# Performance work log

Measured on AMD Instinct MI355X. Metric: run time of the kernel, lower is better.

Reference implementation:

```python
import jax, jax.numpy as jnp
import numpy as np

B, S, D = 2, 2048, 4096
H, KVH, HD = 32, 8, 128
N_REP = H // KVH
ROPE_THETA = 10000.0


def setup_inputs() -> dict:
    key = jax.random.key(0)
    ks = jax.random.split(key, 6)
    x_norm = jax.random.normal(ks[0], (B, S, D), dtype=jnp.float32)
    scale = 0.02
    wq = jax.random.normal(ks[1], (H * HD, D), dtype=jnp.float32) * scale
    wk = jax.random.normal(ks[2], (KVH * HD, D), dtype=jnp.float32) * scale
    wv = jax.random.normal(ks[3], (KVH * HD, D), dtype=jnp.float32) * scale
    wo = jax.random.normal(ks[4], (D, H * HD), dtype=jnp.float32) * scale
    # RoPE tables: freqs_cis[t, j] = exp(i * t * theta^{-2j/HD})
    inv_freq = 1.0 / (ROPE_THETA ** (jnp.arange(0, HD, 2, dtype=jnp.float32) / HD))  # [HD/2]
    angles = jnp.arange(S, dtype=jnp.float32)[:, None] * inv_freq[None, :]  # [S, HD/2]
    freqs_cos = jnp.cos(angles)
    freqs_sin = jnp.sin(angles)
    # causal additive mask (0 on/below diagonal, -1e9 above)
    mask = jnp.where(jnp.arange(S)[None, :] > jnp.arange(S)[:, None], jnp.float32(-1e9), jnp.float32(0.0))
    return {"x_norm": x_norm, "wq": wq, "wk": wk, "wv": wv, "wo": wo,
            "freqs_cos": freqs_cos, "freqs_sin": freqs_sin, "mask": mask, "start_pos": 0}


def _apply_rope(t, cos, sin):
    # t: [B, S, h, HD]; cos/sin: [S, HD/2] -> rotate consecutive pairs
    tr = t.reshape(*t.shape[:-1], HD // 2, 2)
    t0, t1 = tr[..., 0], tr[..., 1]
    c = cos[None, :, None, :]
    s = sin[None, :, None, :]
    out = jnp.stack([t0 * c - t1 * s, t0 * s + t1 * c], axis=-1)
    return out.reshape(t.shape)


def reference(x_norm, wq, wk, wv, wo, freqs_cos, freqs_sin, mask, start_pos):
    # QKV projections (torch Linear: y = x @ W.T)
    xq = jnp.einsum("bsd,ed->bse", x_norm, wq).reshape(B, S, H, HD)
    xk = jnp.einsum("bsd,ed->bse", x_norm, wk).reshape(B, S, KVH, HD)
    xv = jnp.einsum("bsd,ed->bse", x_norm, wv).reshape(B, S, KVH, HD)
    xq = _apply_rope(xq, freqs_cos, freqs_sin)
    xk = _apply_rope(xk, freqs_cos, freqs_sin)
    # start_pos == 0 prefill: cache slice [:start_pos+seqlen] == freshly written xk/xv
    keys = jnp.repeat(xk, N_REP, axis=2)    # [B, S, H, HD] (GQA repeat_kv)
    values = jnp.repeat(xv, N_REP, axis=2)  # [B, S, H, HD]
    scale = 1.0 / np.sqrt(HD).astype(np.float32)
    scores = jnp.einsum("bqhd,bkhd->bhqk", xq, keys) * scale
    scores = scores + mask[None, None, :, :]
    probs = jax.nn.softmax(scores.astype(jnp.float32), axis=-1).astype(xq.dtype)
    out = jnp.einsum("bhqk,bkhd->bqhd", probs, values).reshape(B, S, H * HD)
    return jnp.einsum("bse,de->bsd", out, wo)
```

## Files before the change

kernel.cpp:

```cpp
#include <hip/hip_runtime.h>
#include <stdint.h>

#define B_N 2
#define S_N 2048
#define D_N 4096
#define H_N 32
#define KVH_N 8
#define HD_N 128
#define NQT (S_N / 64)
#define QS_LOG2E 0.12751743f

typedef __attribute__((ext_vector_type(8))) short bf16x8;
typedef __attribute__((ext_vector_type(4))) float f32x4;

__device__ __forceinline__ unsigned short f2bf(float f) {
    union { float f; unsigned u; } v; v.f = f;
    unsigned u = v.u;
    u += 0x7fffu + ((u >> 16) & 1u);
    return (unsigned short)(u >> 16);
}
__device__ __forceinline__ float bf2f(unsigned short h) {
    union { unsigned u; float f; } v; v.u = ((unsigned)h) << 16;
    return v.f;
}
__device__ __forceinline__ unsigned cvt_pk_bf16(float lo, float hi) {
    unsigned r;
    asm("v_cvt_pk_bf16_f32 %0, %1, %2" : "=v"(r) : "v"(lo), "v"(hi));
    return r;
}

__device__ __forceinline__ void gl16(const unsigned short* g, unsigned short* l) {
    __builtin_amdgcn_global_load_lds(
        (const __attribute__((address_space(1))) void*)g,
        (__attribute__((address_space(3))) void*)l, 16, 0, 0);
}

__global__ void __launch_bounds__(256) conv_f32_bf16(const float* __restrict__ in,
                                                     unsigned short* __restrict__ out) {
    int i = (blockIdx.x * 256 + threadIdx.x) * 4;
    float4 v = *(const float4*)(in + i);
    ushort4 o;
    o.x = f2bf(v.x); o.y = f2bf(v.y); o.z = f2bf(v.z); o.w = f2bf(v.w);
    *(ushort4*)(out + i) = o;
}

template<int HEADS, int STRIDE>
__global__ void __launch_bounds__(256) rope_kernel(unsigned short* __restrict__ t,
                                                   const float* __restrict__ cosb,
                                                   const float* __restrict__ sinb,
                                                   float scale) {
    int p = blockIdx.x * 256 + threadIdx.x;
    int i = p & 63;
    int hr = p >> 6;
    int m = hr / HEADS;
    int hh = hr - m * HEADS;
    int s = m & (S_N - 1);
    size_t off = (size_t)m * STRIDE + hh * HD_N + 2 * i;
    unsigned v = *(const unsigned*)(t + off);
    float t0 = bf2f((unsigned short)(v & 0xffffu));
    float t1 = bf2f((unsigned short)(v >> 16));
    float c = cosb[s * 64 + i], sn = sinb[s * 64 + i];
    float o0 = (t0 * c - t1 * sn) * scale;
    float o1 = (t0 * sn + t1 * c) * scale;
    *(unsigned*)(t + off) = (unsigned)f2bf(o0) | ((unsigned)f2bf(o1) << 16);
}

#define BAR() __builtin_amdgcn_s_barrier()
#define VMC4() asm volatile("s_waitcnt vmcnt(4)" ::: "memory")

#define STG(SRC, LDSBUF, H, T) do {                                         \
        int kk_ = ((T) * 64) & kmask;                                       \
        gl16(SRC[(H)*2 + 0] + kk_, &LDSBUF[((H)*2 + 0) * 4096 + dstoff]);   \
        gl16(SRC[(H)*2 + 1] + kk_, &LDSBUF[((H)*2 + 1) * 4096 + dstoff]);   \
    } while (0)

template<int F32OUT>
__global__ void __launch_bounds__(512, 2)
gemm256(const unsigned short* __restrict__ A, const unsigned short* __restrict__ Bm,
        void* __restrict__ Cv, int M, int N, int K) {
    __shared__ unsigned short ldsA[2][16384];
    __shared__ unsigned short ldsB[2][16384];

    const int tid = threadIdx.x;
    const int lane = tid & 63;
    const int w = tid >> 6;
    const int li = lane & 15, lg = lane >> 4;
    const int wr = w >> 2, wc = w & 3;

    const int nwg = gridDim.x;
    const int cpx = nwg >> 3;
    const int wg = (blockIdx.x & 7) * cpx + (blockIdx.x >> 3);
    const int nbn = N >> 8;
    const int bm = wg / nbn, bn = wg - bm * nbn;
    const int m0 = bm << 8, n0 = bn << 8;

    const int rbase = ((tid >> 7) << 4) + ((tid >> 2) & 15);
    const int cstg = ((tid >> 6) & 1) * 32 + (((tid & 3) * 8) ^ (((tid >> 5) & 1) << 4));
    const unsigned short* Asrc[4];
    const unsigned short* Bsrc[4];
#pragma unroll
    for (int hj = 0; hj < 4; ++hj) {
        Asrc[hj] = A + (size_t)(m0 + hj * 64 + rbase) * K + cstg;
        Bsrc[hj] = Bm + (size_t)(n0 + hj * 64 + rbase) * K + cstg;
    }
    const int dstoff = tid * 8;
    const int kmask = K - 1;

    f32x4 acc[8][4];
#pragma unroll
    for (int i = 0; i < 8; ++i)
#pragma unroll
        for (int j = 0; j < 4; ++j) acc[i][j] = (f32x4){0.f, 0.f, 0.f, 0.f};

    const int colpart = (lg * 16) ^ ((li >> 3) << 5);

#define LDB(buf) do {                                                        \
        _Pragma("unroll")                                                    \
        for (int ni_ = 0; ni_ < 4; ++ni_) {                                  \
            _Pragma("unroll")                                                \
            for (int ks_ = 0; ks_ < 2; ++ks_)                                \
                bfr[ni_][ks_] = *(const bf16x8*)((const char*)&ldsB[buf][0]  \
                    + (wc * 4 + ni_) * 2048 + ks_ * 1024 + li * 64 + colpart); \
        }                                                                    \
    } while (0)

#define LDA(buf, q) do {                                                     \
        _Pragma("unroll")                                                    \
        for (int m_ = 0; m_ < 2; ++m_) {                                     \
            _Pragma("unroll")                                                \
            for (int ks_ = 0; ks_ < 2; ++ks_)                                \
                af[m_][ks_] = *(const bf16x8*)((const char*)&ldsA[buf][0]    \
                    + (wr * 8 + (q) * 2 + m_) * 2048 + ks_ * 1024 + li * 64 + colpart); \
        }                                                                    \
    } while (0)

#define MFMAQ(q) do {                                                        \
        __builtin_amdgcn_s_setprio(1);                                       \
        _Pragma("unroll")                                                    \
        for (int ks_ = 0; ks_ < 2; ++ks_) {                                  \
            _Pragma("unroll")                                                \
            for (int m_ = 0; m_ < 2; ++m_) {                                 \
                _Pragma("unroll")                                            \
                for (int ni_ = 0; ni_ < 4; ++ni_)                            \
                    acc[(q)*2 + m_][ni_] = __builtin_amdgcn_mfma_f32_16x16x32_bf16( \
                        af[m_][ks_], bfr[ni_][ks_], acc[(q)*2 + m_][ni_], 0, 0, 0); \
            }                                                                \
        }                                                                    \
        __builtin_amdgcn_s_setprio(0);                                       \
    } while (0)

    STG(Asrc, ldsA[0], 0, 0); STG(Asrc, ldsA[0], 1, 0);
    STG(Bsrc, ldsB[0], 0, 0); STG(Bsrc, ldsB[0], 1, 0);
    STG(Bsrc, ldsB[1], 0, 1); STG(Bsrc, ldsB[1], 1, 1);
    VMC4();
    BAR();

    const int NIT = K >> 7;
    bf16x8 bfr[4][2], af[2][2];
#pragma unroll 1
    for (int i = 0; i < NIT; ++i) {
        const int T = 2 * i;
        LDB(0); LDA(0, 0);
        STG(Asrc, ldsA[1], 0, T + 1);
        BAR(); MFMAQ(0); BAR();
        LDA(0, 1);
        STG(Asrc, ldsA[1], 1, T + 1);
        STG(Bsrc, ldsB[0], 0, T + 2);
        BAR(); MFMAQ(1); BAR();
        LDA(0, 2);
        STG(Bsrc, ldsB[0], 1, T + 2);
        BAR(); MFMAQ(2); BAR();
        LDA(0, 3);
        BAR(); MFMAQ(3); VMC4(); BAR();
        LDB(1); LDA(1, 0);
        STG(Asrc, ldsA[0], 0, T + 2);
        BAR(); MFMAQ(0); BAR();
        LDA(1, 1);
        STG(Asrc, ldsA[0], 1, T + 2);
        BAR(); MFMAQ(1); BAR();
        LDA(1, 2);
        STG(Bsrc, ldsB[1], 0, T + 3);
        BAR(); MFMAQ(2); BAR();
        LDA(1, 3);
        STG(Bsrc, ldsB[1], 1, T + 3);
        BAR(); MFMAQ(3); VMC4(); BAR();
    }

    const int r0 = m0 + wr * 128 + lg * 4;
    const int c0 = n0 + wc * 64 + li;
    if (F32OUT) {
        float* C = (float*)Cv;
#pragma unroll
        for (int mi = 0; mi < 8; ++mi)
#pragma unroll
            for (int ni = 0; ni < 4; ++ni)
#pragma unroll
                for (int rr = 0; rr < 4; ++rr)
                    C[(size_t)(r0 + mi * 16 + rr) * N + c0 + ni * 16] = acc[mi][ni][rr];
    } else {
        unsigned short* C = (unsigned short*)Cv;
#pragma unroll
        for (int mi = 0; mi < 8; ++mi)
#pragma unroll
            for (int ni = 0; ni < 4; ++ni)
#pragma unroll
                for (int rr = 0; rr < 4; ++rr)
                    C[(size_t)(r0 + mi * 16 + rr) * N + c0 + ni * 16] = f2bf(acc[mi][ni][rr]);
    }
#undef LDB
#undef LDA
#undef MFMAQ
}


__device__ __forceinline__ void stage_k8(const unsigned short* kt_base,
                                         unsigned short* ks_base, int w, int lane) {
#pragma unroll
    for (int j = 0; j < 2; ++j) {
        int row = (w * 2 + j) * 4 + (lane >> 4);
        int colb = (lane & 15) * 16;
        int key = (row & 7) << 4;
        gl16(kt_base + (size_t)row * 2048 + ((colb ^ key) >> 1),
             ks_base + (w * 2 + j) * 512);
    }
}

__device__ __forceinline__ void load_v(const unsigned short* vt_base, int tid, uint4& a0, uint4& a1) {
    int kv = (tid >> 4) * 2, d0 = (tid & 15) * 8;
    const unsigned short* vp = vt_base + (size_t)kv * 2048 + d0;
    a0 = *(const uint4*)vp;
    a1 = *(const uint4*)(vp + 2048);
}

__device__ __forceinline__ void write_v(unsigned short* vt_lds, int tid, uint4 a0, uint4 a1) {
    int kv = (tid >> 4) * 2, d0 = (tid & 15) * 8;
    union { uint4 q; unsigned short u[8]; } x0, x1;
    x0.q = a0; x1.q = a1;
#pragma unroll
    for (int jj = 0; jj < 8; ++jj) {
        int d = d0 + jj;
        unsigned pack = (unsigned)x0.u[jj] | ((unsigned)x1.u[jj] << 16);
        int key = ((d ^ (d >> 3)) & 7) << 4;
        *(unsigned*)((char*)vt_lds + d * 128 + ((kv * 2) ^ key)) = pack;
    }
}

__global__ void __launch_bounds__(512, 2) attn_kernel(const unsigned short* __restrict__ Q,
                                                      const unsigned short* __restrict__ Kb,
                                                      const unsigned short* __restrict__ Vb,
                                                      unsigned short* __restrict__ O) {
    __shared__ unsigned short Ks[2][64 * 128];
    __shared__ unsigned short Vt[2][128 * 64];

    const int pidx = blockIdx.x;
    const int bg = blockIdx.y;
    const int b = bg >> 3, kvh = bg & 7;
    const int tid = threadIdx.x;
    const int w = tid >> 6, lane = tid & 63;
    const int li = lane & 15, lg = lane >> 4;
    const int h = kvh * 4 + (w >> 1);
    const int qh = (w & 1) * 32;

    const unsigned short* KVrow0 = Kb + (size_t)b * S_N * 2048 + kvh * 128;
    const unsigned short* Vrow0  = Vb + (size_t)b * S_N * 2048 + kvh * 128;

#pragma unroll 1
    for (int pass = 0; pass < 2; ++pass) {
        const int qt = pass ? (NQT - 1 - pidx) : pidx;
        const int nt = qt + 1;

        bf16x8 qf[2][4];
        {
            const unsigned short* qp = Q + ((size_t)b * S_N + qt * 64 + qh + li) * (H_N * HD_N)
                                         + h * HD_N + lg * 8;
#pragma unroll
            for (int mi = 0; mi < 2; ++mi)
#pragma unroll
                for (int ds = 0; ds < 4; ++ds)
                    qf[mi][ds] = *(const bf16x8*)(qp + (size_t)mi * 16 * (H_N * HD_N) + ds * 32);
        }

        float mreg[2], lreg[2];
#pragma unroll
        for (int mi = 0; mi < 2; ++mi) { mreg[mi] = -1e30f; lreg[mi] = 0.f; }
        f32x4 o_acc[2][8];
#pragma unroll
        for (int mi = 0; mi < 2; ++mi)
#pragma unroll
            for (int di = 0; di < 8; ++di) o_acc[mi][di] = (f32x4){0.f, 0.f, 0.f, 0.f};

        {
            stage_k8(KVrow0, &Ks[0][0], w, lane);
            uint4 a0, a1;
            load_v(Vrow0, tid, a0, a1);
            write_v(&Vt[0][0], tid, a0, a1);
        }
        __syncthreads();

#pragma unroll 1
        for (int t = 0; t < nt; ++t) {
            const int c = t & 1;
            const bool pre = (t + 1 < nt);
            uint4 a0, a1;
            if (pre) {
                stage_k8(KVrow0 + (size_t)(t + 1) * 64 * 2048, &Ks[c ^ 1][0], w, lane);
                load_v(Vrow0 + (size_t)(t + 1) * 64 * 2048, tid, a0, a1);
            }

            f32x4 sT[2][4];
#pragma unroll
            for (int mi = 0; mi < 2; ++mi)
#pragma unroll
                for (int ni = 0; ni < 4; ++ni) sT[mi][ni] = (f32x4){0.f, 0.f, 0.f, 0.f};
            __builtin_amdgcn_s_setprio(1);
#pragma unroll
            for (int ni = 0; ni < 4; ++ni) {
                const int kvc = ni * 16 + li;
                const int kkey = (kvc & 7) << 4;
                bf16x8 kf[4];
#pragma unroll
                for (int ds = 0; ds < 4; ++ds)
                    kf[ds] = *(const bf16x8*)((char*)&Ks[c][0] + kvc * 256
                                              + ((ds * 64 + lg * 16) ^ kkey));
#pragma unroll
                for (int mi = 0; mi < 2; ++mi)
#pragma unroll
                    for (int ds = 0; ds < 4; ++ds)
                        sT[mi][ni] = __builtin_amdgcn_mfma_f32_16x16x32_bf16(kf[ds], qf[mi][ds], sT[mi][ni], 0, 0, 0);
            }
            __builtin_amdgcn_s_setprio(0);

            if (t == qt) {
#pragma unroll
                for (int mi = 0; mi < 2; ++mi) {
                    int qq = qh + mi * 16 + li;
#pragma unroll
                    for (int ni = 0; ni < 4; ++ni)
#pragma unroll
                        for (int r = 0; r < 4; ++r)
                            if (ni * 16 + lg * 4 + r > qq) sT[mi][ni][r] = -1e30f;
                }
            }

            float fac0[2];
#pragma unroll
            for (int mi = 0; mi < 2; ++mi) {
                float pm = sT[mi][0][0];
#pragma unroll
                for (int ni = 0; ni < 4; ++ni)
#pragma unroll
                    for (int r = 0; r < 4; ++r) pm = fmaxf(pm, sT[mi][ni][r]);
                pm = fmaxf(pm, __shfl_xor(pm, 16));
                pm = fmaxf(pm, __shfl_xor(pm, 32));
                float mn = fmaxf(mreg[mi], pm);
                fac0[mi] = __builtin_amdgcn_exp2f(mreg[mi] - mn);
                mreg[mi] = mn;
#pragma unroll
                for (int ni = 0; ni < 4; ++ni)
#pragma unroll
                    for (int r = 0; r < 4; ++r)
                        sT[mi][ni][r] = __builtin_amdgcn_exp2f(sT[mi][ni][r] - mn);
                float rs = 0.f;
#pragma unroll
                for (int ni = 0; ni < 4; ++ni)
#pragma unroll
                    for (int r = 0; r < 4; ++r) rs += sT[mi][ni][r];
                rs += __shfl_xor(rs, 16);
                rs += __shfl_xor(rs, 32);
                lreg[mi] = lreg[mi] * fac0[mi] + rs;
            }

#pragma unroll
            for (int mi = 0; mi < 2; ++mi) {
                float facR[4];
#pragma unroll
                for (int rr = 0; rr < 4; ++rr)
                    facR[rr] = __shfl(fac0[mi], (lg << 4) | (lg * 4 + rr));
#pragma unroll
                for (int di = 0; di < 8; ++di)
#pragma unroll
                    for (int rr = 0; rr < 4; ++rr) o_acc[mi][di][rr] *= facR[rr];
            }

            union U { bf16x8 v; unsigned u[4]; };
            U pa[2][2];
#pragma unroll
            for (int mi = 0; mi < 2; ++mi)
#pragma unroll
                for (int ks = 0; ks < 2; ++ks) {
                    pa[mi][ks].u[0] = cvt_pk_bf16(sT[mi][2 * ks][0], sT[mi][2 * ks][1]);
                    pa[mi][ks].u[1] = cvt_pk_bf16(sT[mi][2 * ks][2], sT[mi][2 * ks][3]);
                    pa[mi][ks].u[2] = cvt_pk_bf16(sT[mi][2 * ks + 1][0], sT[mi][2 * ks + 1][1]);
                    pa[mi][ks].u[3] = cvt_pk_bf16(sT[mi][2 * ks + 1][2], sT[mi][2 * ks + 1][3]);
                }

            __builtin_amdgcn_s_setprio(1);
#pragma unroll
            for (int di = 0; di < 8; ++di) {
                int d = di * 16 + li;
                int vkey = ((d ^ (d >> 3)) & 7) << 4;
                const char* vbase = (const char*)&Vt[c][0] + d * 128;
                bf16x8 vf[2];
#pragma unroll
                for (int ks = 0; ks < 2; ++ks) {
                    union { bf16x8 v; unsigned long long g[2]; } vv;
                    int cb = ks * 64 + lg * 8;
                    vv.g[0] = *(const unsigned long long*)(vbase + (cb ^ vkey));
                    vv.g[1] = *(const unsigned long long*)(vbase + ((cb + 32) ^ vkey));
                    vf[ks] = vv.v;
                }
#pragma unroll
                for (int mi = 0; mi < 2; ++mi)
#pragma unroll
                    for (int ks = 0; ks < 2; ++ks)
                        o_acc[mi][di] = __builtin_amdgcn_mfma_f32_16x16x32_bf16(pa[mi][ks].v, vf[ks], o_acc[mi][di], 0, 0, 0);
            }
            __builtin_amdgcn_s_setprio(0);

            if (pre) write_v(&Vt[c ^ 1][0], tid, a0, a1);
            __syncthreads();
        }

        unsigned short* op = O + ((size_t)b * S_N + qt * 64 + qh + lg * 4) * (H_N * HD_N)
                               + h * HD_N + li;
#pragma unroll
        for (int mi = 0; mi < 2; ++mi) {
            float iv = 1.f / lreg[mi];
            float ivR[4];
#pragma unroll
            for (int rr = 0; rr < 4; ++rr)
                ivR[rr] = __shfl(iv, (lg << 4) | (lg * 4 + rr));
#pragma unroll
            for (int di = 0; di < 8; ++di)
#pragma unroll
                for (int rr = 0; rr < 4; ++rr)
                    op[((size_t)(mi * 16 + rr)) * (H_N * HD_N) + di * 16]
                        = f2bf(o_acc[mi][di][rr] * ivR[rr]);
        }
    }
}

extern "C" void kernel_launch(void* const* d_in, const int* in_sizes, int n_in,
                              void* d_out, int out_size, void* d_ws, size_t ws_size,
                              hipStream_t stream) {
    (void)in_sizes; (void)n_in; (void)out_size; (void)ws_size;
    const float* x  = (const float*)d_in[0];
    const float* wq = (const float*)d_in[1];
    const float* wk = (const float*)d_in[2];
    const float* wv = (const float*)d_in[3];
    const float* wo = (const float*)d_in[4];
    const float* fc = (const float*)d_in[5];
    const float* fs = (const float*)d_in[6];
    float* out = (float*)d_out;

    char* ws = (char*)d_ws;
    unsigned short* xb  = (unsigned short*)(ws);
    unsigned short* wb  = (unsigned short*)(ws + 33554432);
    unsigned short* wkv = (unsigned short*)(ws + 67108864);
    unsigned short* Qb  = (unsigned short*)(ws + 83886080);
    unsigned short* KVb = (unsigned short*)(ws + 117440512);

    const int BS = B_N * S_N;

    conv_f32_bf16<<<dim3(BS * D_N / 1024), 256, 0, stream>>>(x, xb);
    conv_f32_bf16<<<dim3(H_N * HD_N * D_N / 1024), 256, 0, stream>>>(wq, wb);
    conv_f32_bf16<<<dim3(KVH_N * HD_N * D_N / 1024), 256, 0, stream>>>(wk, wkv);
    conv_f32_bf16<<<dim3(KVH_N * HD_N * D_N / 1024), 256, 0, stream>>>(wv, wkv + KVH_N * HD_N * D_N);

    gemm256<0><<<dim3((BS / 256) * (D_N / 256)), 512, 0, stream>>>(xb, wb, Qb, BS, D_N, D_N);
    conv_f32_bf16<<<dim3(D_N * H_N * HD_N / 1024), 256, 0, stream>>>(wo, wb);
    gemm256<0><<<dim3((BS / 256) * (2048 / 256)), 512, 0, stream>>>(xb, wkv, KVb, BS, 2048, D_N);

    rope_kernel<H_N, H_N * HD_N><<<dim3(BS * H_N * 64 / 256), 256, 0, stream>>>(Qb, fc, fs, QS_LOG2E);
    rope_kernel<KVH_N, 2 * KVH_N * HD_N><<<dim3(BS * KVH_N * 64 / 256), 256, 0, stream>>>(KVb, fc, fs, 1.0f);

    attn_kernel<<<dim3(NQT / 2, B_N * KVH_N), 512, 0, stream>>>(Qb, KVb, KVb + 1024, Qb);

    gemm256<1><<<dim3((BS / 256) * (D_N / 256)), 512, 0, stream>>>(Qb, wb, out, BS, D_N, D_N);
}
```

Measured before the change: 594.2 us.

## Double-buffer GEMM LDS fragments in registers to overlap reads with MFMA

Restructures the gemm256 main loop so A/B fragments are read from LDS into a second register set while MFMAs run on the first. This removes one of the two barriers per quarter step, so each step has one barrier instead of a barrier before and after the MFMA block. It also replaces the per-row source pointer arrays with a single base pointer plus computed offsets to save registers. The cost is more fragment registers, which may pressure occupancy under the 512x2 launch bounds. It also risks LDS write/read hazards now that fewer barriers separate staging from fragment reads.

```diff
diff --git a/kernel.cpp b/kernel.cpp
--- a/kernel.cpp
+++ b/kernel.cpp
@@ -68,12 +68,6 @@
 #define BAR() __builtin_amdgcn_s_barrier()
 #define VMC4() asm volatile("s_waitcnt vmcnt(4)" ::: "memory")
 
-#define STG(SRC, LDSBUF, H, T) do {                                         \
-        int kk_ = ((T) * 64) & kmask;                                       \
-        gl16(SRC[(H)*2 + 0] + kk_, &LDSBUF[((H)*2 + 0) * 4096 + dstoff]);   \
-        gl16(SRC[(H)*2 + 1] + kk_, &LDSBUF[((H)*2 + 1) * 4096 + dstoff]);   \
-    } while (0)
-
 template<int F32OUT>
 __global__ void __launch_bounds__(512, 2)
 gemm256(const unsigned short* __restrict__ A, const unsigned short* __restrict__ Bm,
@@ -96,13 +90,8 @@
 
     const int rbase = ((tid >> 7) << 4) + ((tid >> 2) & 15);
     const int cstg = ((tid >> 6) & 1) * 32 + (((tid & 3) * 8) ^ (((tid >> 5) & 1) << 4));
-    const unsigned short* Asrc[4];
-    const unsigned short* Bsrc[4];
-#pragma unroll
-    for (int hj = 0; hj < 4; ++hj) {
-        Asrc[hj] = A + (size_t)(m0 + hj * 64 + rbase) * K + cstg;
-        Bsrc[hj] = Bm + (size_t)(n0 + hj * 64 + rbase) * K + cstg;
-    }
+    const unsigned short* Abase = A + (size_t)(m0 + rbase) * K + cstg;
+    const unsigned short* Bbase = Bm + (size_t)(n0 + rbase) * K + cstg;
     const int dstoff = tid * 8;
     const int kmask = K - 1;
 
@@ -114,76 +103,99 @@
 
     const int colpart = (lg * 16) ^ ((li >> 3) << 5);
 
-#define LDB(buf) do {                                                        \
-        _Pragma("unroll")                                                    \
-        for (int ni_ = 0; ni_ < 4; ++ni_) {                                  \
-            _Pragma("unroll")                                                \
-            for (int ks_ = 0; ks_ < 2; ++ks_)                                \
-                bfr[ni_][ks_] = *(const bf16x8*)((const char*)&ldsB[buf][0]  \
-                    + (wc * 4 + ni_) * 2048 + ks_ * 1024 + li * 64 + colpart); \
-        }                                                                    \
+#define STG(BASE, LDSBUF, H, T) do {                                              \
+        int kk_ = ((T) * 64) & kmask;                                             \
+        gl16(BASE + (size_t)(((H) * 2 + 0) * 64) * K + kk_,                       \
+             &LDSBUF[((H) * 2 + 0) * 4096 + dstoff]);                             \
+        gl16(BASE + (size_t)(((H) * 2 + 1) * 64) * K + kk_,                       \
+             &LDSBUF[((H) * 2 + 1) * 4096 + dstoff]);                             \
     } while (0)
 
-#define LDA(buf, q) do {                                                     \
-        _Pragma("unroll")                                                    \
-        for (int m_ = 0; m_ < 2; ++m_) {                                     \
-            _Pragma("unroll")                                                \
-            for (int ks_ = 0; ks_ < 2; ++ks_)                                \
-                af[m_][ks_] = *(const bf16x8*)((const char*)&ldsA[buf][0]    \
+#define LDBs(set, buf) do {                                                       \
+        _Pragma("unroll")                                                         \
+        for (int ni_ = 0; ni_ < 4; ++ni_) {                                       \
+            _Pragma("unroll")                                                     \
+            for (int ks_ = 0; ks_ < 2; ++ks_)                                     \
+                bfr[set][ni_][ks_] = *(const bf16x8*)((const char*)&ldsB[buf][0]  \
+                    + (wc * 4 + ni_) * 2048 + ks_ * 1024 + li * 64 + colpart);    \
+        }                                                                         \
+    } while (0)
+
+#define LDAs(set, buf, q) do {                                                    \
+        _Pragma("unroll")                                                         \
+        for (int m_ = 0; m_ < 2; ++m_) {                                          \
+            _Pragma("unroll")                                                     \
+            for (int ks_ = 0; ks_ < 2; ++ks_)                                     \
+                af[set][m_][ks_] = *(const bf16x8*)((const char*)&ldsA[buf][0]    \
                     + (wr * 8 + (q) * 2 + m_) * 2048 + ks_ * 1024 + li * 64 + colpart); \
-        }                                                                    \
+        }                                                                         \
     } while (0)
 
-#define MFMAQ(q) do {                                                        \
-        __builtin_amdgcn_s_setprio(1);                                       \
-        _Pragma("unroll")                                                    \
-        for (int ks_ = 0; ks_ < 2; ++ks_) {                                  \
-            _Pragma("unroll")                                                \
-            for (int m_ = 0; m_ < 2; ++m_) {                                 \
-                _Pragma("unroll")                                            \
-                for (int ni_ = 0; ni_ < 4; ++ni_)                            \
-                    acc[(q)*2 + m_][ni_] = __builtin_amdgcn_mfma_f32_16x16x32_bf16( \
-                        af[m_][ks_], bfr[ni_][ks_], acc[(q)*2 + m_][ni_], 0, 0, 0); \
-            }                                                                \
-        }                                                                    \
-        __builtin_amdgcn_s_setprio(0);                                       \
+#define MFMAs(sb, sa, q) do {                                                     \
+        __builtin_amdgcn_s_setprio(1);                                            \
+        _Pragma("unroll")                                                         \
+        for (int ks_ = 0; ks_ < 2; ++ks_) {                                       \
+            _Pragma("unroll")                                                     \
+            for (int m_ = 0; m_ < 2; ++m_) {                                      \
+                _Pragma("unroll")                                                 \
+                for (int ni_ = 0; ni_ < 4; ++ni_)                                 \
+                    acc[(q) * 2 + m_][ni_] = __builtin_amdgcn_mfma_f32_16x16x32_bf16( \
+                        af[sa][m_][ks_], bfr[sb][ni_][ks_], acc[(q) * 2 + m_][ni_], 0, 0, 0); \
+            }                                                                     \
+        }                                                                         \
+        __builtin_amdgcn_s_setprio(0);                                            \
     } while (0)
 
-    STG(Asrc, ldsA[0], 0, 0); STG(Asrc, ldsA[0], 1, 0);
-    STG(Bsrc, ldsB[0], 0, 0); STG(Bsrc, ldsB[0], 1, 0);
-    STG(Bsrc, ldsB[1], 0, 1); STG(Bsrc, ldsB[1], 1, 1);
+    STG(Abase, ldsA[0], 0, 0); STG(Abase, ldsA[0], 1, 0);
+    STG(Bbase, ldsB[0], 0, 0); STG(Bbase, ldsB[0], 1, 0);
+    STG(Bbase, ldsB[1], 0, 1); STG(Bbase, ldsB[1], 1, 1);
     VMC4();
     BAR();
 
+    bf16x8 bfr[2][4][2], af[2][2][2];
+    LDBs(0, 0);
+    LDAs(0, 0, 0);
+
     const int NIT = K >> 7;
-    bf16x8 bfr[4][2], af[2][2];
 #pragma unroll 1
     for (int i = 0; i < NIT; ++i) {
         const int T = 2 * i;
-        LDB(0); LDA(0, 0);
-        STG(Asrc, ldsA[1], 0, T + 1);
-        BAR(); MFMAQ(0); BAR();
-        LDA(0, 1);
-        STG(Asrc, ldsA[1], 1, T + 1);
-        STG(Bsrc, ldsB[0], 0, T + 2);
-        BAR(); MFMAQ(1); BAR();
-        LDA(0, 2);
-        STG(Bsrc, ldsB[0], 1, T + 2);
-        BAR(); MFMAQ(2); BAR();
-        LDA(0, 3);
-        BAR(); MFMAQ(3); VMC4(); BAR();
-        LDB(1); LDA(1, 0);
-        STG(Asrc, ldsA[0], 0, T + 2);
-        BAR(); MFMAQ(0); BAR();
-        LDA(1, 1);
-        STG(Asrc, ldsA[0], 1, T + 2);
-        BAR(); MFMAQ(1); BAR();
-        LDA(1, 2);
-        STG(Bsrc, ldsB[1], 0, T + 3);
-        BAR(); MFMAQ(2); BAR();
-        LDA(1, 3);
-        STG(Bsrc, ldsB[1], 1, T + 3);
-        BAR(); MFMAQ(3); VMC4(); BAR();
+        LDAs(1, 0, 1);
+        STG(Abase, ldsA[1], 0, T + 1);
+        MFMAs(0, 0, 0);
+        BAR();
+        LDAs(0, 0, 2);
+        STG(Abase, ldsA[1], 1, T + 1);
+        STG(Bbase, ldsB[0], 0, T + 2);
+        MFMAs(0, 1, 1);
+        BAR();
+        LDAs(1, 0, 3);
+        STG(Bbase, ldsB[0], 1, T + 2);
+        MFMAs(0, 0, 2);
+        VMC4();
+        BAR();
+        LDBs(1, 1);
+        LDAs(0, 1, 0);
+        MFMAs(0, 1, 3);
+        BAR();
+        LDAs(1, 1, 1);
+        STG(Abase, ldsA[0], 0, T + 2);
+        MFMAs(1, 0, 0);
+        BAR();
+        LDAs(0, 1, 2);
+        STG(Abase, ldsA[0], 1, T + 2);
+        STG(Bbase, ldsB[1], 0, T + 3);
+        MFMAs(1, 1, 1);
+        BAR();
+        LDAs(1, 1, 3);
+        STG(Bbase, ldsB[1], 1, T + 3);
+        MFMAs(1, 0, 2);
+        VMC4();
+        BAR();
+        LDBs(0, 0);
+        LDAs(0, 0, 0);
+        MFMAs(1, 1, 3);
+        BAR();
     }
 
     const int r0 = m0 + wr * 128 + lg * 4;
@@ -207,11 +219,11 @@
                 for (int rr = 0; rr < 4; ++rr)
                     C[(size_t)(r0 + mi * 16 + rr) * N + c0 + ni * 16] = f2bf(acc[mi][ni][rr]);
     }
-#undef LDB
-#undef LDA
-#undef MFMAQ
-}
-
+#undef STG
+#undef LDBs
+#undef LDAs
+#undef MFMAs
+}
 
 __device__ __forceinline__ void stage_k8(const unsigned short* kt_base,
                                          unsigned short* ks_base, int w, int lane) {
```

After: 579.8 us. 1.02x faster.
